# Kernel tuning notes

Measured on AMD Instinct MI355X. Metric: run time of the kernel, lower is better.

Reference implementation:

```python
import jax, jax.numpy as jnp
import numpy as np

CODE_DIM = 512
NUM_CODEBOOKS = 4
CODEBOOK_SIZE = 1024
SUB_DIM = CODE_DIM // NUM_CODEBOOKS


def setup_inputs() -> dict:
    key = jax.random.key(0)
    k1, k2 = jax.random.split(key)
    z_e = jax.random.normal(k1, (64, 512, CODE_DIM), dtype=jnp.float32)
    bound = 1.0 / CODEBOOK_SIZE
    codebooks = jax.random.uniform(
        k2, (NUM_CODEBOOKS, CODEBOOK_SIZE, SUB_DIM),
        minval=-bound, maxval=bound, dtype=jnp.float32)
    return {"z_e": z_e, "codebooks": codebooks}


def reference(z_e, codebooks):
    B, L, D = z_e.shape
    K, S, d = codebooks.shape  # K codebooks, S entries, sub_dim d
    N = B * L
    flat = z_e.reshape(N, K, d)  # per-codebook sub-vectors
    # squared euclidean distances: [N, K, S]
    dist = ((flat ** 2).sum(-1)[:, :, None]
            - 2.0 * jnp.einsum('nkd,ksd->nks', flat, codebooks)
            + (codebooks ** 2).sum(-1)[None, :, :])
    idx = jnp.argmin(dist, axis=-1)  # [N, K]
    # gather nearest codes per codebook
    z_q = codebooks[jnp.arange(K)[None, :], idx]  # [N, K, d]
    z_q_all = z_q.reshape(B, L, D)
    # sum_k mse_k / K == mean over the full concatenated tensor
    codebook_loss = jnp.mean((z_q_all - jax.lax.stop_gradient(z_e)) ** 2)
    commit_loss = jnp.mean((z_e - jax.lax.stop_gradient(z_q_all)) ** 2)
    # perplexity via index counts (no NxS one-hot materialization)
    counts = jnp.zeros((K, S), dtype=z_e.dtype).at[
        jnp.broadcast_to(jnp.arange(K)[None, :], idx.shape), idx].add(1.0)
    avg_probs = counts / N  # [K, S]
    perplexity = jnp.exp(
        -(avg_probs * jnp.log(jnp.clip(avg_probs, 1e-8))).sum(-1)).mean()
    z_q_st = z_e + jax.lax.stop_gradient(z_q_all - z_e)
    indices_all = idx.reshape(B, L, K)
    return indices_all, z_q_st, z_q_all, codebook_loss, commit_loss, perplexity
```

## Files before the change

### kernel.cpp

```cpp
#include <hip/hip_runtime.h>
#include <math.h>

#define NVEC  32768
#define DDIM  512
#define KCB   4
#define SCB   1024
#define SUBD  128

#define IDX_COUNT (NVEC * KCB)
#define ZQ_COUNT  (NVEC * DDIM)
#define OFF_ZQ_ST  IDX_COUNT
#define OFF_ZQ_ALL (IDX_COUNT + ZQ_COUNT)
#define OFF_SCAL   (IDX_COUNT + 2 * ZQ_COUNT)


typedef _Float16 v2h __attribute__((ext_vector_type(2)));
typedef _Float16 f16x8 __attribute__((ext_vector_type(8)));
typedef float f32x16 __attribute__((ext_vector_type(16)));
union U32H2 { unsigned int u; v2h h; };

__device__ __forceinline__ float fmul(float a, float b) { return __fmul_rn(a, b); }
__device__ __forceinline__ float fadd(float a, float b) { return __fadd_rn(a, b); }
__device__ __forceinline__ float fsub(float a, float b) { return __fsub_rn(a, b); }

__device__ __forceinline__ float np_dot128(const float* __restrict__ u,
                                           const float* __restrict__ v) {
  float r[8];
#pragma unroll
  for (int j = 0; j < 8; ++j) r[j] = fmul(u[j], v[j]);
#pragma unroll
  for (int i = 8; i < 128; i += 8) {
#pragma unroll
    for (int j = 0; j < 8; ++j) r[j] = fadd(r[j], fmul(u[i + j], v[i + j]));
  }
  return fadd(fadd(fadd(r[0], r[1]), fadd(r[2], r[3])),
              fadd(fadd(r[4], r[5]), fadd(r[6], r[7])));
}

__global__ __launch_bounds__(256) void k_convert(
    const float* __restrict__ cb, unsigned int* __restrict__ cb16,
    float* __restrict__ c2s) {
  const int wave = blockIdx.x * 4 + (threadIdx.x >> 6);
  const int lane = threadIdx.x & 63;
  for (int i = 0; i < 16; ++i) {
    const int code = wave * 16 + i;
    const float2 v = ((const float2*)(cb + (size_t)code * SUBD))[lane];
    float tot = fmaf(v.x, v.x, v.y * v.y);
#pragma unroll
    for (int off = 32; off > 0; off >>= 1) tot += __shfl_down(tot, off, 64);
    v2h h; h.x = (_Float16)(v.x * 1024.0f); h.y = (_Float16)(v.y * 1024.0f);
    U32H2 t; t.h = h;
    cb16[(size_t)code * 64 + lane] = t.u;
    if (lane == 0) c2s[code] = tot * 1048576.0f;
  }
}

__global__ __launch_bounds__(256) void k_c2np(const float* __restrict__ cb,
                                              float* __restrict__ c2np) {
  const int c = blockIdx.x * 256 + threadIdx.x;
  const float* row = cb + (size_t)c * SUBD;
  c2np[c] = np_dot128(row, row);
}

#define SCORE_HALF(ACC, STOFF)                                             \
  {                                                                        \
    _Pragma("unroll")                                                      \
    for (int g = 0; g < 4; ++g) {                                          \
      const float4 cv = *(const float4*)(c2b + (STOFF) + hi * 4 + g * 8);  \
      const float ca[4] = {cv.x, cv.y, cv.z, cv.w};                        \
      _Pragma("unroll")                                                    \
      for (int r = 0; r < 4; ++r) {                                        \
        const float score = fmaf(-2048.0f, (ACC)[g * 4 + r], ca[r]);       \
        const int s = tb + (STOFF) + hi * 4 + g * 8 + r;                   \
        if (score < m3) {                                                  \
          if (score < m0)      { m3=m2;i3=i2; m2=m1;i2=i1; m1=m0;i1=i0; m0=score;i0=s; } \
          else if (score < m1) { m3=m2;i3=i2; m2=m1;i2=i1; m1=score;i1=s; } \
          else if (score < m2) { m3=m2;i3=i2; m2=score;i2=s; }             \
          else                 { m3=score;i3=s; }                          \
        }                                                                  \
      }                                                                    \
    }                                                                      \
  }

__global__ __launch_bounds__(256) void k_scan(
    const float* __restrict__ z_e, const unsigned int* __restrict__ cb16,
    const float* __restrict__ c2s, unsigned short* __restrict__ cand) {
  const int tid = threadIdx.x;
  const int lane = tid & 63;
  const int w = tid >> 6;
  const int hi = lane >> 5;
  const int ml = lane & 31;
  const int k = blockIdx.y;
  const int n = blockIdx.x * 128 + w * 32 + ml;

  __shared__ __align__(16) unsigned int ctile[2][4096];
  __shared__ __align__(16) float c2l[SCB];

  const uint4* gk = (const uint4*)cb16 + (size_t)k * SCB * 16;
  const int rbase = tid >> 4;
  const int ss = (tid & 15) ^ rbase;

  f16x8 xf[8];
  {
    const float* xp = z_e + (size_t)n * DDIM + k * SUBD + hi * 8;
#pragma unroll
    for (int ks = 0; ks < 8; ++ks) {
      const float4 a = *(const float4*)(xp + ks * 16);
      const float4 b = *(const float4*)(xp + ks * 16 + 4);
      f16x8 h;
      h[0] = (_Float16)a.x; h[1] = (_Float16)a.y;
      h[2] = (_Float16)a.z; h[3] = (_Float16)a.w;
      h[4] = (_Float16)b.x; h[5] = (_Float16)b.y;
      h[6] = (_Float16)b.z; h[7] = (_Float16)b.w;
      xf[ks] = h;
    }
  }

  for (int i = tid; i < SCB; i += 256) c2l[i] = c2s[k * SCB + i];
  {
    uint4* dst = (uint4*)ctile[0];
#pragma unroll
    for (int p = 0; p < 4; ++p)
      dst[p * 256 + tid] = gk[(p * 16 + rbase) * 16 + ss];
  }
  __syncthreads();

  float m0 = 1e30f, m1 = 1e30f, m2 = 1e30f, m3 = 1e30f;
  int i0 = 0, i1 = 0, i2 = 0, i3 = 0;

  for (int tile = 0; tile < 16; ++tile) {
    uint4 pf0, pf1, pf2, pf3;
    if (tile < 15) {
      const uint4* gt = gk + (size_t)(tile + 1) * 1024;
      pf0 = gt[(0 * 16 + rbase) * 16 + ss];
      pf1 = gt[(1 * 16 + rbase) * 16 + ss];
      pf2 = gt[(2 * 16 + rbase) * 16 + ss];
      pf3 = gt[(3 * 16 + rbase) * 16 + ss];
    }

    const unsigned char* bufb = (const unsigned char*)ctile[tile & 1];
    f32x16 acc0, acc1;
#pragma unroll
    for (int z = 0; z < 16; ++z) { acc0[z] = 0.0f; acc1[z] = 0.0f; }

#pragma unroll
    for (int ks = 0; ks < 8; ++ks) {
      const int phys = (((ks * 2 + hi) ^ (lane & 15)) << 4);
      const f16x8 a0 = *(const f16x8*)(bufb + ml * 256 + phys);
      const f16x8 a1 = *(const f16x8*)(bufb + (ml + 32) * 256 + phys);
      acc0 = __builtin_amdgcn_mfma_f32_32x32x16_f16(a0, xf[ks], acc0, 0, 0, 0);
      acc1 = __builtin_amdgcn_mfma_f32_32x32x16_f16(a1, xf[ks], acc1, 0, 0, 0);
    }

    const int tb = tile * 64;
    const float* c2b = c2l + tb;
    SCORE_HALF(acc0, 0)
    SCORE_HALF(acc1, 32)

    if (tile < 15) {
      uint4* dst = (uint4*)ctile[(tile + 1) & 1];
      dst[0 * 256 + tid] = pf0;
      dst[1 * 256 + tid] = pf1;
      dst[2 * 256 + tid] = pf2;
      dst[3 * 256 + tid] = pf3;
    }
    __syncthreads();
  }

  const unsigned long long pk =
      (unsigned long long)(unsigned short)i0 |
      ((unsigned long long)(unsigned short)i1 << 16) |
      ((unsigned long long)(unsigned short)i2 << 32) |
      ((unsigned long long)(unsigned short)i3 << 48);
  *(unsigned long long*)(cand + ((size_t)(n * KCB + k)) * 8 + hi * 4) = pk;
}

__global__ __launch_bounds__(256) void k_merge(
    const float* __restrict__ z_e, const float* __restrict__ cb,
    const unsigned short* __restrict__ cand, const float* __restrict__ c2np,
    float* __restrict__ out_idx, int* __restrict__ counts) {
  const int g = blockIdx.x * 256 + threadIdx.x;
  const int n = g >> 2, k = g & 3;

  float4 xv[32];
  const float4* xp = (const float4*)(z_e + (size_t)n * DDIM + k * SUBD);
#pragma unroll
  for (int j = 0; j < 32; ++j) xv[j] = xp[j];
  const float* xs = (const float*)xv;
  const float A = np_dot128(xs, xs);

  const unsigned short* cp = cand + (size_t)g * 8;
  float bd = 1e30f;
  int bi = SCB;
#pragma unroll
  for (int t = 0; t < 8; ++t) {
    const int s = cp[t];
    const float* c = cb + (size_t)(k * SCB + s) * SUBD;
    const float E = np_dot128(xs, c);
    const float dist = fadd(fsub(A, fmul(2.0f, E)), c2np[k * SCB + s]);
    if (dist < bd || (dist == bd && s < bi)) { bd = dist; bi = s; }
  }

  out_idx[g] = (float)bi;
  atomicAdd(&counts[k * SCB + bi], 1);
}

__global__ __launch_bounds__(256) void k_perp(const int* __restrict__ counts,
                                              float* __restrict__ out_perp) {
  const int w = threadIdx.x >> 6;
  const int lane = threadIdx.x & 63;
  double h = 0.0;
  for (int i = 0; i < SCB / 64; ++i) {
    const int cnt = counts[w * SCB + i * 64 + lane];
    if (cnt > 0) {
      const double p = (double)cnt * (1.0 / 32768.0);
      h += p * log(p);
    }
  }
#pragma unroll
  for (int off = 32; off > 0; off >>= 1) h += __shfl_down(h, off, 64);
  __shared__ double hs[4];
  if (lane == 0) hs[w] = h;
  __syncthreads();
  if (threadIdx.x == 0) {
    double perp = 0.0;
    for (int w2 = 0; w2 < 4; ++w2) perp += exp(-hs[w2]);
    out_perp[0] = (float)(perp * 0.25);
  }
}

__global__ __launch_bounds__(256) void k_gather(
    const float* __restrict__ z_e, const float* __restrict__ cb,
    const float* __restrict__ idxf, float* __restrict__ zq_st,
    float* __restrict__ zq_all, float* __restrict__ loss_acc) {
  const int base = blockIdx.x * 4096;
  float local = 0.f;
#pragma unroll
  for (int i = 0; i < 16; ++i) {
    const int q = base + i * 256 + threadIdx.x;
    const int nn = q >> 7;
    const int rem = q & 127;
    const int kk = rem >> 5;
    const int j4 = rem & 31;
    const int idx = (int)idxf[nn * KCB + kk];
    const float4 v = ((const float4*)cb)[(size_t)(kk * SCB + idx) * 32 + j4];
    ((float4*)zq_st)[q] = v;
    ((float4*)zq_all)[q] = v;
    const float4 z = ((const float4*)z_e)[q];
    const float dx = z.x - v.x, dy = z.y - v.y, dz = z.z - v.z, dw = z.w - v.w;
    local += dx * dx + dy * dy + dz * dz + dw * dw;
  }
#pragma unroll
  for (int off = 32; off > 0; off >>= 1) local += __shfl_down(local, off, 64);
  __shared__ float red[4];
  const int w = threadIdx.x >> 6, lane = threadIdx.x & 63;
  if (lane == 0) red[w] = local;
  __syncthreads();
  if (threadIdx.x == 0) atomicAdd(loss_acc, (red[0] + red[1]) + (red[2] + red[3]));
}

__global__ void k_scal(float* __restrict__ scal) {
  if (threadIdx.x == 0) {
    const float m = scal[0] * (1.0f / 16777216.0f);
    scal[0] = m;
    scal[1] = m;
  }
}

extern "C" void kernel_launch(void* const* d_in, const int* in_sizes, int n_in,
                              void* d_out, int out_size, void* d_ws, size_t ws_size,
                              hipStream_t stream) {
  const float* z_e = (const float*)d_in[0];
  const float* cb = (const float*)d_in[1];
  float* out = (float*)d_out;

  float* zq_all = out + OFF_ZQ_ALL;
  int* counts = (int*)zq_all;
  float* c2s = zq_all + 4096;
  float* c2np = zq_all + 8192;
  unsigned int* cb16 = (unsigned int*)(zq_all + 12288);
  unsigned short* cand = (unsigned short*)(zq_all + 274432);
  float* scal = out + OFF_SCAL;

  hipMemsetAsync(counts, 0, KCB * SCB * sizeof(int), stream);
  hipMemsetAsync(scal, 0, 3 * sizeof(float), stream);

  k_convert<<<64, 256, 0, stream>>>(cb, cb16, c2s);
  k_c2np<<<16, 256, 0, stream>>>(cb, c2np);
  dim3 gs(NVEC / 128, KCB);
  k_scan<<<gs, 256, 0, stream>>>(z_e, cb16, c2s, cand);
  k_merge<<<IDX_COUNT / 256, 256, 0, stream>>>(z_e, cb, cand, c2np, out, counts);
  k_perp<<<1, 256, 0, stream>>>(counts, scal + 2);
  k_gather<<<1024, 256, 0, stream>>>(z_e, cb, out, out + OFF_ZQ_ST, zq_all, scal);
  k_scal<<<1, 64, 0, stream>>>(scal);
}
```

Baseline: 414.5 us.

## Fuse prep/perplexity/loss kernels and use branchless packed-key top-4 in scan

Merges the memsets, codebook conversion and norm kernels into one prep kernel. The perplexity and loss finalisation move into the merge kernel through a last-block atomic counter, and the loss is taken from the best distance instead of being recomputed in gather, so gather no longer reads z_e. The scan kernel replaces its branchy float top-4 insertion with a branchless min/max network on integer keys that pack the truncated score with the index. It also reads c2 norms directly from global memory instead of shared memory and sets an occupancy hint. Truncating the score to an integer could alter candidate selection, and summing fp32 distances for the loss may lose precision.

```diff
diff --git a/kernel.cpp b/kernel.cpp
--- a/kernel.cpp
+++ b/kernel.cpp
@@ -37,9 +37,29 @@
               fadd(fadd(r[4], r[5]), fadd(r[6], r[7])));
 }
 
-__global__ __launch_bounds__(256) void k_convert(
+__device__ __forceinline__ int imin(int a, int b) { return a < b ? a : b; }
+__device__ __forceinline__ int imax(int a, int b) { return a > b ? a : b; }
+
+__device__ __forceinline__ void ins4(int& k0, int& k1, int& k2, int& k3, int x) {
+  int a = imax(k0, x); k0 = imin(k0, x);
+  int b = imax(k1, a); k1 = imin(k1, a);
+  int c = imax(k2, b); k2 = imin(k2, b);
+  k3 = imin(k3, c);
+}
+
+__global__ __launch_bounds__(256) void k_prep(
     const float* __restrict__ cb, unsigned int* __restrict__ cb16,
-    float* __restrict__ c2s) {
+    float* __restrict__ c2s, float* __restrict__ c2np,
+    int* __restrict__ counts, float* __restrict__ scal,
+    int* __restrict__ ctrs) {
+  const int gt = blockIdx.x * 256 + threadIdx.x;
+  if (gt < KCB * SCB) counts[gt] = 0;
+  if (gt < 3) scal[gt] = 0.0f;
+  if (gt < 2) ctrs[gt] = 0;
+  if (gt < KCB * SCB) {
+    const float* row = cb + (size_t)gt * SUBD;
+    c2np[gt] = np_dot128(row, row);
+  }
   const int wave = blockIdx.x * 4 + (threadIdx.x >> 6);
   const int lane = threadIdx.x & 63;
   for (int i = 0; i < 16; ++i) {
@@ -55,34 +75,22 @@
   }
 }
 
-__global__ __launch_bounds__(256) void k_c2np(const float* __restrict__ cb,
-                                              float* __restrict__ c2np) {
-  const int c = blockIdx.x * 256 + threadIdx.x;
-  const float* row = cb + (size_t)c * SUBD;
-  c2np[c] = np_dot128(row, row);
-}
-
-#define SCORE_HALF(ACC, STOFF)                                             \
-  {                                                                        \
-    _Pragma("unroll")                                                      \
-    for (int g = 0; g < 4; ++g) {                                          \
-      const float4 cv = *(const float4*)(c2b + (STOFF) + hi * 4 + g * 8);  \
-      const float ca[4] = {cv.x, cv.y, cv.z, cv.w};                        \
-      _Pragma("unroll")                                                    \
-      for (int r = 0; r < 4; ++r) {                                        \
-        const float score = fmaf(-2048.0f, (ACC)[g * 4 + r], ca[r]);       \
-        const int s = tb + (STOFF) + hi * 4 + g * 8 + r;                   \
-        if (score < m3) {                                                  \
-          if (score < m0)      { m3=m2;i3=i2; m2=m1;i2=i1; m1=m0;i1=i0; m0=score;i0=s; } \
-          else if (score < m1) { m3=m2;i3=i2; m2=m1;i2=i1; m1=score;i1=s; } \
-          else if (score < m2) { m3=m2;i3=i2; m2=score;i2=s; }             \
-          else                 { m3=score;i3=s; }                          \
-        }                                                                  \
-      }                                                                    \
-    }                                                                      \
-  }
-
-__global__ __launch_bounds__(256) void k_scan(
+#define SCORE(ACC, STOFF, K0, K1, K2, K3)                                    \
+  {                                                                          \
+    _Pragma("unroll")                                                        \
+    for (int g = 0; g < 4; ++g) {                                            \
+      const float4 cv = *(const float4*)(c2b + (STOFF) + hi * 4 + g * 8);    \
+      const float ca[4] = {cv.x, cv.y, cv.z, cv.w};                          \
+      _Pragma("unroll")                                                      \
+      for (int r = 0; r < 4; ++r) {                                          \
+        const float sc = fmaf(-2048.0f, (ACC)[g * 4 + r], ca[r]);            \
+        const int key = ((int)sc << 10) | (tb + (STOFF) + hi * 4 + g * 8 + r); \
+        ins4(K0, K1, K2, K3, key);                                           \
+      }                                                                      \
+    }                                                                        \
+  }
+
+__global__ __launch_bounds__(256, 4) void k_scan(
     const float* __restrict__ z_e, const unsigned int* __restrict__ cb16,
     const float* __restrict__ c2s, unsigned short* __restrict__ cand) {
   const int tid = threadIdx.x;
@@ -94,9 +102,9 @@
   const int n = blockIdx.x * 128 + w * 32 + ml;
 
   __shared__ __align__(16) unsigned int ctile[2][4096];
-  __shared__ __align__(16) float c2l[SCB];
 
   const uint4* gk = (const uint4*)cb16 + (size_t)k * SCB * 16;
+  const float* c2k = c2s + k * SCB;
   const int rbase = tid >> 4;
   const int ss = (tid & 15) ^ rbase;
 
@@ -116,26 +124,24 @@
     }
   }
 
-  for (int i = tid; i < SCB; i += 256) c2l[i] = c2s[k * SCB + i];
+  uint4 pf[4];
+#pragma unroll
+  for (int p = 0; p < 4; ++p) pf[p] = gk[(p * 16 + rbase) * 16 + ss];
   {
     uint4* dst = (uint4*)ctile[0];
 #pragma unroll
-    for (int p = 0; p < 4; ++p)
-      dst[p * 256 + tid] = gk[(p * 16 + rbase) * 16 + ss];
+    for (int p = 0; p < 4; ++p) dst[p * 256 + tid] = pf[p];
   }
   __syncthreads();
 
-  float m0 = 1e30f, m1 = 1e30f, m2 = 1e30f, m3 = 1e30f;
-  int i0 = 0, i1 = 0, i2 = 0, i3 = 0;
+  int kA0 = 0x7FFFFFFF, kA1 = 0x7FFFFFFF, kA2 = 0x7FFFFFFF, kA3 = 0x7FFFFFFF;
+  int kB0 = 0x7FFFFFFF, kB1 = 0x7FFFFFFF, kB2 = 0x7FFFFFFF, kB3 = 0x7FFFFFFF;
 
   for (int tile = 0; tile < 16; ++tile) {
-    uint4 pf0, pf1, pf2, pf3;
     if (tile < 15) {
       const uint4* gt = gk + (size_t)(tile + 1) * 1024;
-      pf0 = gt[(0 * 16 + rbase) * 16 + ss];
-      pf1 = gt[(1 * 16 + rbase) * 16 + ss];
-      pf2 = gt[(2 * 16 + rbase) * 16 + ss];
-      pf3 = gt[(3 * 16 + rbase) * 16 + ss];
+#pragma unroll
+      for (int p = 0; p < 4; ++p) pf[p] = gt[(p * 16 + rbase) * 16 + ss];
     }
 
     const unsigned char* bufb = (const unsigned char*)ctile[tile & 1];
@@ -153,34 +159,40 @@
     }
 
     const int tb = tile * 64;
-    const float* c2b = c2l + tb;
-    SCORE_HALF(acc0, 0)
-    SCORE_HALF(acc1, 32)
+    const float* c2b = c2k + tb;
+    SCORE(acc0, 0, kA0, kA1, kA2, kA3)
+    SCORE(acc1, 32, kB0, kB1, kB2, kB3)
 
     if (tile < 15) {
       uint4* dst = (uint4*)ctile[(tile + 1) & 1];
-      dst[0 * 256 + tid] = pf0;
-      dst[1 * 256 + tid] = pf1;
-      dst[2 * 256 + tid] = pf2;
-      dst[3 * 256 + tid] = pf3;
+#pragma unroll
+      for (int p = 0; p < 4; ++p) dst[p * 256 + tid] = pf[p];
     }
     __syncthreads();
   }
 
+  ins4(kA0, kA1, kA2, kA3, kB0);
+  ins4(kA0, kA1, kA2, kA3, kB1);
+  ins4(kA0, kA1, kA2, kA3, kB2);
+  ins4(kA0, kA1, kA2, kA3, kB3);
+
   const unsigned long long pk =
-      (unsigned long long)(unsigned short)i0 |
-      ((unsigned long long)(unsigned short)i1 << 16) |
-      ((unsigned long long)(unsigned short)i2 << 32) |
-      ((unsigned long long)(unsigned short)i3 << 48);
+      (unsigned long long)(unsigned short)(kA0 & 1023) |
+      ((unsigned long long)(unsigned short)(kA1 & 1023) << 16) |
+      ((unsigned long long)(unsigned short)(kA2 & 1023) << 32) |
+      ((unsigned long long)(unsigned short)(kA3 & 1023) << 48);
   *(unsigned long long*)(cand + ((size_t)(n * KCB + k)) * 8 + hi * 4) = pk;
 }
 
 __global__ __launch_bounds__(256) void k_merge(
     const float* __restrict__ z_e, const float* __restrict__ cb,
     const unsigned short* __restrict__ cand, const float* __restrict__ c2np,
-    float* __restrict__ out_idx, int* __restrict__ counts) {
-  const int g = blockIdx.x * 256 + threadIdx.x;
+    float* __restrict__ out_idx, int* __restrict__ counts,
+    float* __restrict__ scal, int* __restrict__ ctrs) {
+  const int tid = threadIdx.x;
+  const int g = blockIdx.x * 256 + tid;
   const int n = g >> 2, k = g & 3;
+  const int w = tid >> 6, lane = tid & 63;
 
   float4 xv[32];
   const float4* xp = (const float4*)(z_e + (size_t)n * DDIM + k * SUBD);
@@ -203,38 +215,54 @@
 
   out_idx[g] = (float)bi;
   atomicAdd(&counts[k * SCB + bi], 1);
-}
-
-__global__ __launch_bounds__(256) void k_perp(const int* __restrict__ counts,
-                                              float* __restrict__ out_perp) {
-  const int w = threadIdx.x >> 6;
-  const int lane = threadIdx.x & 63;
-  double h = 0.0;
-  for (int i = 0; i < SCB / 64; ++i) {
-    const int cnt = counts[w * SCB + i * 64 + lane];
-    if (cnt > 0) {
-      const double p = (double)cnt * (1.0 / 32768.0);
-      h += p * log(p);
-    }
-  }
-#pragma unroll
-  for (int off = 32; off > 0; off >>= 1) h += __shfl_down(h, off, 64);
-  __shared__ double hs[4];
-  if (lane == 0) hs[w] = h;
+
+  float local = bd;
+#pragma unroll
+  for (int off = 32; off > 0; off >>= 1) local += __shfl_down(local, off, 64);
+  __shared__ float red[4];
+  if (lane == 0) red[w] = local;
   __syncthreads();
-  if (threadIdx.x == 0) {
-    double perp = 0.0;
-    for (int w2 = 0; w2 < 4; ++w2) perp += exp(-hs[w2]);
-    out_perp[0] = (float)(perp * 0.25);
+
+  __shared__ int lastf;
+  if (tid == 0) {
+    atomicAdd(&scal[0], (red[0] + red[1]) + (red[2] + red[3]));
+    __threadfence();
+    lastf = (atomicAdd(&ctrs[0], 1) == (int)gridDim.x - 1);
+  }
+  __syncthreads();
+
+  if (lastf) {
+    double h = 0.0;
+    for (int i = 0; i < SCB / 64; ++i) {
+      const int cnt = __hip_atomic_load(&counts[w * SCB + i * 64 + lane],
+                                        __ATOMIC_RELAXED, __HIP_MEMORY_SCOPE_AGENT);
+      if (cnt > 0) {
+        const double p = (double)cnt * (1.0 / 32768.0);
+        h += p * log(p);
+      }
+    }
+#pragma unroll
+    for (int off = 32; off > 0; off >>= 1) h += __shfl_down(h, off, 64);
+    __shared__ double hs[4];
+    if (lane == 0) hs[w] = h;
+    __syncthreads();
+    if (tid == 0) {
+      double perp = 0.0;
+      for (int w2 = 0; w2 < 4; ++w2) perp += exp(-hs[w2]);
+      scal[2] = (float)(perp * 0.25);
+      const float L = __hip_atomic_load(&scal[0], __ATOMIC_RELAXED,
+                                        __HIP_MEMORY_SCOPE_AGENT);
+      const float m = L * (1.0f / 16777216.0f);
+      scal[0] = m;
+      scal[1] = m;
+    }
   }
 }
 
 __global__ __launch_bounds__(256) void k_gather(
-    const float* __restrict__ z_e, const float* __restrict__ cb,
-    const float* __restrict__ idxf, float* __restrict__ zq_st,
-    float* __restrict__ zq_all, float* __restrict__ loss_acc) {
+    const float* __restrict__ cb, const float* __restrict__ idxf,
+    float* __restrict__ zq_st, float* __restrict__ zq_all) {
   const int base = blockIdx.x * 4096;
-  float local = 0.f;
 #pragma unroll
   for (int i = 0; i < 16; ++i) {
     const int q = base + i * 256 + threadIdx.x;
@@ -246,24 +274,6 @@
     const float4 v = ((const float4*)cb)[(size_t)(kk * SCB + idx) * 32 + j4];
     ((float4*)zq_st)[q] = v;
     ((float4*)zq_all)[q] = v;
-    const float4 z = ((const float4*)z_e)[q];
-    const float dx = z.x - v.x, dy = z.y - v.y, dz = z.z - v.z, dw = z.w - v.w;
-    local += dx * dx + dy * dy + dz * dz + dw * dw;
-  }
-#pragma unroll
-  for (int off = 32; off > 0; off >>= 1) local += __shfl_down(local, off, 64);
-  __shared__ float red[4];
-  const int w = threadIdx.x >> 6, lane = threadIdx.x & 63;
-  if (lane == 0) red[w] = local;
-  __syncthreads();
-  if (threadIdx.x == 0) atomicAdd(loss_acc, (red[0] + red[1]) + (red[2] + red[3]));
-}
-
-__global__ void k_scal(float* __restrict__ scal) {
-  if (threadIdx.x == 0) {
-    const float m = scal[0] * (1.0f / 16777216.0f);
-    scal[0] = m;
-    scal[1] = m;
   }
 }
 
@@ -280,17 +290,13 @@
   float* c2np = zq_all + 8192;
   unsigned int* cb16 = (unsigned int*)(zq_all + 12288);
   unsigned short* cand = (unsigned short*)(zq_all + 274432);
+  int* ctrs = (int*)(zq_all + 800000);
   float* scal = out + OFF_SCAL;
 
-  hipMemsetAsync(counts, 0, KCB * SCB * sizeof(int), stream);
-  hipMemsetAsync(scal, 0, 3 * sizeof(float), stream);
-
-  k_convert<<<64, 256, 0, stream>>>(cb, cb16, c2s);
-  k_c2np<<<16, 256, 0, stream>>>(cb, c2np);
+  k_prep<<<64, 256, 0, stream>>>(cb, cb16, c2s, c2np, counts, scal, ctrs);
   dim3 gs(NVEC / 128, KCB);
   k_scan<<<gs, 256, 0, stream>>>(z_e, cb16, c2s, cand);
-  k_merge<<<IDX_COUNT / 256, 256, 0, stream>>>(z_e, cb, cand, c2np, out, counts);
-  k_perp<<<1, 256, 0, stream>>>(counts, scal + 2);
-  k_gather<<<1024, 256, 0, stream>>>(z_e, cb, out, out + OFF_ZQ_ST, zq_all, scal);
-  k_scal<<<1, 64, 0, stream>>>(scal);
-}
+  k_merge<<<IDX_COUNT / 256, 256, 0, stream>>>(z_e, cb, cand, c2np, out, counts,
+                                               scal, ctrs);
+  k_gather<<<1024, 256, 0, stream>>>(cb, out, out + OFF_ZQ_ST, zq_all);
+}
```

Measured after the change: 386.1 us. 1.07x faster.
